# Kernel tuning notes

Measured on AMD Instinct MI355X. Metric: run time of the kernel, lower is better.

## Reference

```python
import jax, jax.numpy as jnp
import numpy as np


def setup_inputs() -> dict:
    key = jax.random.key(0)
    k1, k2 = jax.random.split(key)
    B, C, H, W = 16, 256, 64, 64
    return {
        "x1": jax.random.normal(k1, (B, C, H, W), dtype=jnp.float32),
        "x2": jax.random.normal(k2, (B, C, H, W), dtype=jnp.float32),
        "k": 256,
    }


def reference(x1, x2, k):
    # concat along channels: [B, 2C, H, W]
    x = jnp.concatenate([x1, x2], axis=1)
    # adaptive avgpool to (1,1) == global mean over H,W -> [B, C_tot]
    pooled = jnp.mean(x, axis=(2, 3))
    # torch.topk(pooled, num_channels) == full descending sort indices
    idx = jnp.argsort(-pooled, axis=1)  # [B, C_tot]
    # gather channels in descending pooled-mean order
    xr = jnp.take_along_axis(x, idx[:, :, None, None], axis=1)  # [B, C_tot, H, W]
    # sum trailing channels [k:] and fold into channel k-1
    tail = jnp.sum(xr[:, k:, :, :], axis=1)  # [B, H, W]
    out = xr[:, :k, :, :].at[:, k - 1, :, :].add(tail)
    return out
```

## Files before the change

### kernel.cpp

```cpp
#include <hip/hip_runtime.h>

#define B   16
#define C1  256
#define C2  512
#define HW  4096
#define TCHUNK 32
#define CPB 8
#define QSPLIT 8

typedef float vf4 __attribute__((ext_vector_type(4)));

__device__ __forceinline__ const vf4* chan_base(
    const float* __restrict__ x1, const float* __restrict__ x2, int b, int c)
{
    return (const vf4*)((c < C1) ? (x1 + (size_t)(b * C1 + c) * HW)
                                 : (x2 + (size_t)(b * C1 + (c - C1)) * HW));
}

__global__ __launch_bounds__(256, 1) void pool_kernel(
    const float* __restrict__ x1, const float* __restrict__ x2,
    float* __restrict__ pooled)
{
    int g  = blockIdx.x * 256 + threadIdx.x;
    int cg = g >> 3;
    int q  = g & 7;
    int b  = cg >> 9;
    int ch = cg & (C2 - 1);
    const vf4* p = chan_base(x1, x2, b, ch) + q * 128;

    vf4 a0 = (vf4)(0.f), a1 = (vf4)(0.f), a2 = (vf4)(0.f), a3 = (vf4)(0.f);
    vf4 a4 = (vf4)(0.f), a5 = (vf4)(0.f), a6 = (vf4)(0.f), a7 = (vf4)(0.f);
    #pragma unroll
    for (int i = 0; i < 128; i += 8) {
        a0 += p[i + 0]; a1 += p[i + 1]; a2 += p[i + 2]; a3 += p[i + 3];
        a4 += p[i + 4]; a5 += p[i + 5]; a6 += p[i + 6]; a7 += p[i + 7];
    }
    vf4 a = ((a0 + a1) + (a2 + a3)) + ((a4 + a5) + (a6 + a7));
    float s = (a.x + a.y) + (a.z + a.w);

    s += __shfl_down(s, 4, 8);
    s += __shfl_down(s, 2, 8);
    s += __shfl_down(s, 1, 8);
    if (q == 0)
        pooled[cg] = s;
}

__global__ __launch_bounds__(512) void sort_kernel(
    const float* __restrict__ pooled, int* __restrict__ idx)
{
    int b = blockIdx.x;
    int t = threadIdx.x;
    __shared__ float sp[C2];
    float v = pooled[b * C2 + t];
    sp[t] = v;
    __syncthreads();
    int rank = 0;
    for (int j = 0; j < C2; ++j) {
        float u = sp[j];
        rank += (u > v) || (u == v && j < t);
    }
    idx[b * C2 + rank] = t;
}

__global__ __launch_bounds__(256) void gather_kernel(
    const float* __restrict__ x1, const float* __restrict__ x2,
    const int* __restrict__ idx, float* __restrict__ out, int k)
{
    int t   = threadIdx.x;
    int bid = blockIdx.x;
    int ntail = B * TCHUNK;

    if (bid < ntail) {
        int b     = bid / TCHUNK;
        int chunk = bid % TCHUNK;
        int g     = t >> 5;
        int slot  = t & 31;
        int off   = chunk * 32 + slot;
        int ntc   = C2 - (k - 1);

        __shared__ int ch[C2];
        __shared__ vf4 red[8][32];
        for (int i = t; i < ntc; i += 256)
            ch[i] = idx[b * C2 + (k - 1) + i];
        __syncthreads();

        vf4 a0 = (vf4)(0.f), a1 = (vf4)(0.f), a2 = (vf4)(0.f), a3 = (vf4)(0.f);
        int j = g;
        for (; j + 24 < ntc; j += 32) {
            int c0 = ch[j], c1 = ch[j + 8], c2 = ch[j + 16], c3 = ch[j + 24];
            a0 += chan_base(x1, x2, b, c0)[off];
            a1 += chan_base(x1, x2, b, c1)[off];
            a2 += chan_base(x1, x2, b, c2)[off];
            a3 += chan_base(x1, x2, b, c3)[off];
        }
        for (; j < ntc; j += 8)
            a0 += chan_base(x1, x2, b, ch[j])[off];

        red[g][slot] = (a0 + a1) + (a2 + a3);
        __syncthreads();
        if (g == 0) {
            vf4 r = (vf4)(0.f);
            #pragma unroll
            for (int gg = 0; gg < 8; ++gg)
                r += red[gg][slot];
            vf4* o = (vf4*)(out + (size_t)(b * k + (k - 1)) * HW);
            o[off] = r;
        }
    } else {
        int cb = bid - ntail;
        int nslots = B * (k - 1);
        int cc[CPB];
        #pragma unroll
        for (int i = 0; i < CPB; ++i) {
            int sl = cb * CPB + i;
            if (sl < nslots) {
                int b = sl / (k - 1);
                int o = sl % (k - 1);
                cc[i] = b * C2 + o;
            } else cc[i] = -1;
        }
        #pragma unroll
        for (int i = 0; i < CPB; ++i)
            if (cc[i] >= 0) cc[i] = idx[cc[i]] | ((cc[i] / C2) << 16);
        #pragma unroll
        for (int i = 0; i < CPB; ++i) {
            if (cc[i] < 0) continue;
            int b = cc[i] >> 16;
            int c = cc[i] & 0xFFFF;
            int sl = cb * CPB + i;
            int o  = sl % (k - 1);
            const vf4* src = chan_base(x1, x2, b, c);
            vf4* dst = (vf4*)(out + (size_t)(b * k + o) * HW);
            vf4 v0 = src[t], v1 = src[t + 256], v2 = src[t + 512], v3 = src[t + 768];
            dst[t] = v0; dst[t + 256] = v1; dst[t + 512] = v2; dst[t + 768] = v3;
        }
    }
}

extern "C" void kernel_launch(void* const* d_in, const int* in_sizes, int n_in,
                              void* d_out, int out_size, void* d_ws, size_t ws_size,
                              hipStream_t stream)
{
    const float* x1 = (const float*)d_in[0];
    const float* x2 = (const float*)d_in[1];
    float* out = (float*)d_out;

    int k = out_size / (B * HW);

    float* pooled = (float*)d_ws;
    int*   idx    = (int*)((char*)d_ws + B * C2 * sizeof(float));

    pool_kernel<<<(B * C2 * QSPLIT) / 256, 256, 0, stream>>>(x1, x2, pooled);
    sort_kernel<<<B, 512, 0, stream>>>(pooled, idx);

    int ncopy = (B * (k - 1) + CPB - 1) / CPB;
    gather_kernel<<<B * TCHUNK + ncopy, 256, 0, stream>>>(x1, x2, idx, out, k);
}
```

Before: 73.69 us.

## Compute tail channel sum as total minus head sum to avoid rereading tail

The pooling pass now also produces a per-pixel sum over all channels and per-chunk channel partial sums. The output pass copies only the top k-1 channels and derives the folded channel as total minus the sum of copied channels. This removes the second read of the tail channels. In exchange the reduce kernel does heavier shuffle work, and the subtraction can introduce floating-point cancellation error.

```diff
diff --git a/kernel.cpp b/kernel.cpp
--- a/kernel.cpp
+++ b/kernel.cpp
@@ -5,8 +5,6 @@
 #define C2  512
 #define HW  4096
 #define TCHUNK 32
-#define CPB 8
-#define QSPLIT 8
 
 typedef float vf4 __attribute__((ext_vector_type(4)));
 
@@ -17,41 +15,72 @@
                                  : (x2 + (size_t)(b * C1 + (c - C1)) * HW));
 }
 
-__global__ __launch_bounds__(256, 1) void pool_kernel(
+__global__ __launch_bounds__(256) void reduce_kernel(
     const float* __restrict__ x1, const float* __restrict__ x2,
-    float* __restrict__ pooled)
+    float* __restrict__ total,
+    float* __restrict__ partials)
 {
-    int g  = blockIdx.x * 256 + threadIdx.x;
-    int cg = g >> 3;
-    int q  = g & 7;
-    int b  = cg >> 9;
-    int ch = cg & (C2 - 1);
-    const vf4* p = chan_base(x1, x2, b, ch) + q * 128;
+    int bid   = blockIdx.x;
+    int b     = bid / TCHUNK;
+    int chunk = bid % TCHUNK;
+    int t     = threadIdx.x;
+    int g     = t >> 5;
+    int slot  = t & 31;
+    int off   = chunk * 32 + slot;
 
-    vf4 a0 = (vf4)(0.f), a1 = (vf4)(0.f), a2 = (vf4)(0.f), a3 = (vf4)(0.f);
-    vf4 a4 = (vf4)(0.f), a5 = (vf4)(0.f), a6 = (vf4)(0.f), a7 = (vf4)(0.f);
-    #pragma unroll
-    for (int i = 0; i < 128; i += 8) {
-        a0 += p[i + 0]; a1 += p[i + 1]; a2 += p[i + 2]; a3 += p[i + 3];
-        a4 += p[i + 4]; a5 += p[i + 5]; a6 += p[i + 6]; a7 += p[i + 7];
+    float* pp = partials + (size_t)(b * TCHUNK + chunk) * C2;
+
+    vf4 t0 = (vf4)(0.f), t1 = (vf4)(0.f), t2 = (vf4)(0.f), t3 = (vf4)(0.f);
+
+    for (int j = 0; j < 64; j += 4) {
+        int c0 = (j + 0) * 8 + g, c1 = (j + 1) * 8 + g;
+        int c2 = (j + 2) * 8 + g, c3 = (j + 3) * 8 + g;
+        vf4 v0 = chan_base(x1, x2, b, c0)[off];
+        vf4 v1 = chan_base(x1, x2, b, c1)[off];
+        vf4 v2 = chan_base(x1, x2, b, c2)[off];
+        vf4 v3 = chan_base(x1, x2, b, c3)[off];
+        t0 += v0; t1 += v1; t2 += v2; t3 += v3;
+
+        float h0 = (v0.x + v0.y) + (v0.z + v0.w);
+        float h1 = (v1.x + v1.y) + (v1.z + v1.w);
+        float h2 = (v2.x + v2.y) + (v2.z + v2.w);
+        float h3 = (v3.x + v3.y) + (v3.z + v3.w);
+        #pragma unroll
+        for (int s = 16; s > 0; s >>= 1) {
+            h0 += __shfl_down(h0, s, 32);
+            h1 += __shfl_down(h1, s, 32);
+            h2 += __shfl_down(h2, s, 32);
+            h3 += __shfl_down(h3, s, 32);
+        }
+        if (slot == 0) {
+            pp[c0] = h0; pp[c1] = h1; pp[c2] = h2; pp[c3] = h3;
+        }
     }
-    vf4 a = ((a0 + a1) + (a2 + a3)) + ((a4 + a5) + (a6 + a7));
-    float s = (a.x + a.y) + (a.z + a.w);
 
-    s += __shfl_down(s, 4, 8);
-    s += __shfl_down(s, 2, 8);
-    s += __shfl_down(s, 1, 8);
-    if (q == 0)
-        pooled[cg] = s;
+    __shared__ vf4 red[8][32];
+    red[g][slot] = (t0 + t1) + (t2 + t3);
+    __syncthreads();
+    if (g == 0) {
+        vf4 r = (vf4)(0.f);
+        #pragma unroll
+        for (int gg = 0; gg < 8; ++gg)
+            r += red[gg][slot];
+        ((vf4*)(total + (size_t)b * HW))[off] = r;
+    }
 }
 
 __global__ __launch_bounds__(512) void sort_kernel(
-    const float* __restrict__ pooled, int* __restrict__ idx)
+    const float* __restrict__ partials, int* __restrict__ idx)
 {
     int b = blockIdx.x;
     int t = threadIdx.x;
+    const float* pp = partials + (size_t)b * TCHUNK * C2 + t;
+    float v = 0.f;
+    #pragma unroll
+    for (int ch = 0; ch < TCHUNK; ++ch)
+        v += pp[ch * C2];
+
     __shared__ float sp[C2];
-    float v = pooled[b * C2 + t];
     sp[t] = v;
     __syncthreads();
     int rank = 0;
@@ -62,78 +91,57 @@
     idx[b * C2 + rank] = t;
 }
 
-__global__ __launch_bounds__(256) void gather_kernel(
+__global__ __launch_bounds__(256) void output_kernel(
     const float* __restrict__ x1, const float* __restrict__ x2,
-    const int* __restrict__ idx, float* __restrict__ out, int k)
+    const int* __restrict__ idx, const float* __restrict__ total,
+    float* __restrict__ out, int k)
 {
-    int t   = threadIdx.x;
-    int bid = blockIdx.x;
-    int ntail = B * TCHUNK;
+    int bid   = blockIdx.x;
+    int b     = bid / TCHUNK;
+    int chunk = bid % TCHUNK;
+    int t     = threadIdx.x;
+    int g     = t >> 5;
+    int slot  = t & 31;
+    int off   = chunk * 32 + slot;
+    int nh    = k - 1;
 
-    if (bid < ntail) {
-        int b     = bid / TCHUNK;
-        int chunk = bid % TCHUNK;
-        int g     = t >> 5;
-        int slot  = t & 31;
-        int off   = chunk * 32 + slot;
-        int ntc   = C2 - (k - 1);
+    __shared__ int ch[C2 / 2];
+    __shared__ vf4 red[8][32];
+    for (int i = t; i < nh; i += 256)
+        ch[i] = idx[b * C2 + i];
+    __syncthreads();
 
-        __shared__ int ch[C2];
-        __shared__ vf4 red[8][32];
-        for (int i = t; i < ntc; i += 256)
-            ch[i] = idx[b * C2 + (k - 1) + i];
-        __syncthreads();
+    vf4 a0 = (vf4)(0.f), a1 = (vf4)(0.f), a2 = (vf4)(0.f), a3 = (vf4)(0.f);
+    const size_t ob = (size_t)b * k;
+    int r = g;
+    for (; r + 24 < nh; r += 32) {
+        int c0 = ch[r], c1 = ch[r + 8], c2 = ch[r + 16], c3 = ch[r + 24];
+        vf4 v0 = chan_base(x1, x2, b, c0)[off];
+        vf4 v1 = chan_base(x1, x2, b, c1)[off];
+        vf4 v2 = chan_base(x1, x2, b, c2)[off];
+        vf4 v3 = chan_base(x1, x2, b, c3)[off];
+        ((vf4*)(out + (ob + r     ) * HW))[off] = v0;
+        ((vf4*)(out + (ob + r +  8) * HW))[off] = v1;
+        ((vf4*)(out + (ob + r + 16) * HW))[off] = v2;
+        ((vf4*)(out + (ob + r + 24) * HW))[off] = v3;
+        a0 += v0; a1 += v1; a2 += v2; a3 += v3;
+    }
+    for (; r < nh; r += 8) {
+        int c0 = ch[r];
+        vf4 v0 = chan_base(x1, x2, b, c0)[off];
+        ((vf4*)(out + (ob + r) * HW))[off] = v0;
+        a0 += v0;
+    }
 
-        vf4 a0 = (vf4)(0.f), a1 = (vf4)(0.f), a2 = (vf4)(0.f), a3 = (vf4)(0.f);
-        int j = g;
-        for (; j + 24 < ntc; j += 32) {
-            int c0 = ch[j], c1 = ch[j + 8], c2 = ch[j + 16], c3 = ch[j + 24];
-            a0 += chan_base(x1, x2, b, c0)[off];
-            a1 += chan_base(x1, x2, b, c1)[off];
-            a2 += chan_base(x1, x2, b, c2)[off];
-            a3 += chan_base(x1, x2, b, c3)[off];
-        }
-        for (; j < ntc; j += 8)
-            a0 += chan_base(x1, x2, b, ch[j])[off];
-
-        red[g][slot] = (a0 + a1) + (a2 + a3);
-        __syncthreads();
-        if (g == 0) {
-            vf4 r = (vf4)(0.f);
-            #pragma unroll
-            for (int gg = 0; gg < 8; ++gg)
-                r += red[gg][slot];
-            vf4* o = (vf4*)(out + (size_t)(b * k + (k - 1)) * HW);
-            o[off] = r;
-        }
-    } else {
-        int cb = bid - ntail;
-        int nslots = B * (k - 1);
-        int cc[CPB];
+    red[g][slot] = (a0 + a1) + (a2 + a3);
+    __syncthreads();
+    if (g == 0) {
+        vf4 hsum = (vf4)(0.f);
         #pragma unroll
-        for (int i = 0; i < CPB; ++i) {
-            int sl = cb * CPB + i;
-            if (sl < nslots) {
-                int b = sl / (k - 1);
-                int o = sl % (k - 1);
-                cc[i] = b * C2 + o;
-            } else cc[i] = -1;
-        }
-        #pragma unroll
-        for (int i = 0; i < CPB; ++i)
-            if (cc[i] >= 0) cc[i] = idx[cc[i]] | ((cc[i] / C2) << 16);
-        #pragma unroll
-        for (int i = 0; i < CPB; ++i) {
-            if (cc[i] < 0) continue;
-            int b = cc[i] >> 16;
-            int c = cc[i] & 0xFFFF;
-            int sl = cb * CPB + i;
-            int o  = sl % (k - 1);
-            const vf4* src = chan_base(x1, x2, b, c);
-            vf4* dst = (vf4*)(out + (size_t)(b * k + o) * HW);
-            vf4 v0 = src[t], v1 = src[t + 256], v2 = src[t + 512], v3 = src[t + 768];
-            dst[t] = v0; dst[t + 256] = v1; dst[t + 512] = v2; dst[t + 768] = v3;
-        }
+        for (int gg = 0; gg < 8; ++gg)
+            hsum += red[gg][slot];
+        vf4 tt = ((const vf4*)(total + (size_t)b * HW))[off];
+        ((vf4*)(out + (ob + (k - 1)) * HW))[off] = tt - hsum;
     }
 }
 
@@ -147,12 +155,11 @@
 
     int k = out_size / (B * HW);
 
-    float* pooled = (float*)d_ws;
-    int*   idx    = (int*)((char*)d_ws + B * C2 * sizeof(float));
+    int*   idx      = (int*)d_ws;
+    float* total    = (float*)((char*)d_ws + B * C2 * sizeof(int));
+    float* partials = total + (size_t)B * HW;
 
-    pool_kernel<<<(B * C2 * QSPLIT) / 256, 256, 0, stream>>>(x1, x2, pooled);
-    sort_kernel<<<B, 512, 0, stream>>>(pooled, idx);
-
-    int ncopy = (B * (k - 1) + CPB - 1) / CPB;
-    gather_kernel<<<B * TCHUNK + ncopy, 256, 0, stream>>>(x1, x2, idx, out, k);
+    reduce_kernel<<<B * TCHUNK, 256, 0, stream>>>(x1, x2, total, partials);
+    sort_kernel<<<B, 512, 0, stream>>>(partials, idx);
+    output_kernel<<<B * TCHUNK, 256, 0, stream>>>(x1, x2, idx, total, out, k);
 }
```

After: 63.90 us. 13.3% less time.
